# Optimization experiments

Measured on AMD Instinct MI355X. Metric: run time of the kernel, lower is better.

## Reference

```python
import jax, jax.numpy as jnp
import numpy as np

# XORChainModel.forward: state[0] = inputs[0]; state[i] = state[i-1] ^ inputs[i]
# i.e. a cumulative XOR (inclusive prefix scan with XOR) along the chain axis.
# XOR is associative, so we use jax.lax.associative_scan (log-depth parallel scan).

SEQ_LEN = 4096  # number of steps in the XOR chain (len(inputs) list in torch)
BITS = 8192     # self.bits: width of each bit vector


def setup_inputs() -> dict:
    key = jax.random.key(0)
    # inputs[i] is a 1-D bit vector of length BITS; stack the whole list into [S, BITS]
    inputs = jax.random.randint(key, (SEQ_LEN, BITS), 0, 2, dtype=jnp.int32)
    return {"inputs": inputs}


def reference(inputs):
    # outputs[i] = inputs[0] ^ inputs[1] ^ ... ^ inputs[i]
    # Equivalent to the torch module's list of per-step states, stacked on axis 0.
    return jax.lax.associative_scan(jnp.bitwise_xor, inputs, axis=0)
```

## Files before the change

kernel.cpp:

```cpp
#include <hip/hip_runtime.h>


#define S 4096
#define B4 2048
#define CHUNK 32
#define NCHUNK (S / CHUNK)
#define TPB 256
#define NCT (B4 / TPB)

typedef unsigned int v4u __attribute__((ext_vector_type(4)));

__global__ __launch_bounds__(TPB) void xor_chunk_total(
        const v4u* __restrict__ in, v4u* __restrict__ ws) {
    const int colg  = blockIdx.x * TPB + threadIdx.x;
    const int chunk = blockIdx.y;
    const v4u* p = in + (size_t)chunk * CHUNK * B4 + colg;
    v4u acc = (v4u){0u, 0u, 0u, 0u};
#pragma unroll 16
    for (int r = 0; r < CHUNK; ++r) {
        acc ^= p[(size_t)r * B4];
    }
    ws[(size_t)chunk * B4 + colg] = acc;
}

__global__ __launch_bounds__(TPB) void xor_scan_out(
        const v4u* __restrict__ in, const v4u* __restrict__ ws,
        v4u* __restrict__ out) {
    const int colg  = blockIdx.x * TPB + threadIdx.x;
    const int chunk = (NCHUNK - 1) - blockIdx.y;

    v4u excl = (v4u){0u, 0u, 0u, 0u};
#pragma unroll 8
    for (int c = 0; c < chunk; ++c) {
        excl ^= ws[(size_t)c * B4 + colg];
    }

    const v4u* p = in  + (size_t)chunk * CHUNK * B4 + colg;
    v4u*       q = out + (size_t)chunk * CHUNK * B4 + colg;
    v4u acc = excl;
#pragma unroll 8
    for (int r = 0; r < CHUNK; ++r) {
        acc ^= p[(size_t)r * B4];
        __builtin_nontemporal_store(acc, &q[(size_t)r * B4]);
    }
}

extern "C" void kernel_launch(void* const* d_in, const int* in_sizes, int n_in,
                              void* d_out, int out_size, void* d_ws, size_t ws_size,
                              hipStream_t stream) {
    const v4u* in = (const v4u*)d_in[0];
    v4u* out = (v4u*)d_out;
    v4u* ws  = (v4u*)d_ws;

    dim3 grid(NCT, NCHUNK);
    xor_chunk_total<<<grid, TPB, 0, stream>>>(in, ws);
    xor_scan_out<<<grid, TPB, 0, stream>>>(in, ws, out);
}
```

Measured before the change: 247.3 us.

## Fuse chunk-total and scan passes into one cooperative kernel with grid sync

Merges the two kernels (per-chunk XOR totals, then prefix and output) into a single cooperative launch separated by a grid-wide barrier. The grid is 8x128 = 1024 blocks of 256 threads, which must all be co-resident; launch bounds request 4 blocks per CU to make that possible. This removes one kernel launch and gap, and may let the second pass re-read input that is still in cache. In exchange it adds the grid-sync cost, the reversed chunk order of the old second kernel is dropped, and if residency is insufficient the cooperative launch fails.

```diff
diff --git a/kernel.cpp b/kernel.cpp
--- a/kernel.cpp
+++ b/kernel.cpp
@@ -1,4 +1,7 @@
 #include <hip/hip_runtime.h>
+#include <hip/hip_cooperative_groups.h>
+
+namespace cg = cooperative_groups;
 
 
 #define S 4096
@@ -7,13 +10,17 @@
 #define NCHUNK (S / CHUNK)
 #define TPB 256
 #define NCT (B4 / TPB)
+#define NBLK (NCHUNK * NCT)
 
 typedef unsigned int v4u __attribute__((ext_vector_type(4)));
 
-__global__ __launch_bounds__(TPB) void xor_chunk_total(
-        const v4u* __restrict__ in, v4u* __restrict__ ws) {
-    const int colg  = blockIdx.x * TPB + threadIdx.x;
+__global__ __launch_bounds__(TPB, 4) void xor_scan_coop(
+        const v4u* __restrict__ in, v4u* __restrict__ out,
+        v4u* __restrict__ ws) {
+    const int ct    = blockIdx.x;
     const int chunk = blockIdx.y;
+    const int colg  = ct * TPB + threadIdx.x;
+
     const v4u* p = in + (size_t)chunk * CHUNK * B4 + colg;
     v4u acc = (v4u){0u, 0u, 0u, 0u};
 #pragma unroll 16
@@ -21,13 +28,8 @@
         acc ^= p[(size_t)r * B4];
     }
     ws[(size_t)chunk * B4 + colg] = acc;
-}
 
-__global__ __launch_bounds__(TPB) void xor_scan_out(
-        const v4u* __restrict__ in, const v4u* __restrict__ ws,
-        v4u* __restrict__ out) {
-    const int colg  = blockIdx.x * TPB + threadIdx.x;
-    const int chunk = (NCHUNK - 1) - blockIdx.y;
+    cg::this_grid().sync();
 
     v4u excl = (v4u){0u, 0u, 0u, 0u};
 #pragma unroll 8
@@ -35,13 +37,11 @@
         excl ^= ws[(size_t)c * B4 + colg];
     }
 
-    const v4u* p = in  + (size_t)chunk * CHUNK * B4 + colg;
-    v4u*       q = out + (size_t)chunk * CHUNK * B4 + colg;
-    v4u acc = excl;
+    v4u* q = out + (size_t)chunk * CHUNK * B4 + colg;
 #pragma unroll 8
     for (int r = 0; r < CHUNK; ++r) {
-        acc ^= p[(size_t)r * B4];
-        __builtin_nontemporal_store(acc, &q[(size_t)r * B4]);
+        excl ^= p[(size_t)r * B4];
+        __builtin_nontemporal_store(excl, &q[(size_t)r * B4]);
     }
 }
 
@@ -52,7 +52,9 @@
     v4u* out = (v4u*)d_out;
     v4u* ws  = (v4u*)d_ws;
 
+    void* args[] = {(void*)&in, (void*)&out, (void*)&ws};
     dim3 grid(NCT, NCHUNK);
-    xor_chunk_total<<<grid, TPB, 0, stream>>>(in, ws);
-    xor_scan_out<<<grid, TPB, 0, stream>>>(in, ws, out);
+    dim3 block(TPB);
+    hipLaunchCooperativeKernel((const void*)xor_scan_coop, grid, block,
+                               args, 0, stream);
 }
```

Result: slower. 366.7 us (+48.3%).
